# Optimization experiments

Hardware: AMD Instinct MI355X
Metric: run time of the kernel (lower is better)

## Reference

```python
import jax, jax.numpy as jnp
import numpy as np

TEMP = 0.1  # config['dsmax_temperature']


def _dual_softmax(sim):
    return jax.nn.softmax(sim, axis=1) * jax.nn.softmax(sim, axis=2)


def _pool(x, out):
    # AdaptiveAvgPool2d((out,out)) for H,W integer multiples of out
    n, c, h, w = x.shape
    return x.reshape(n, c, out, h // out, out, w // out).mean(axis=(3, 5))


def _conv1x1(w, x):
    # bias-free 1x1 conv: w [O,C], x [N,C,H,W]
    return jnp.einsum('oc,nchw->nohw', w, x)


def setup_inputs() -> dict:
    key = jax.random.key(0)
    ks = jax.random.split(key, 16)
    N = 1
    d = {}
    d['feats12_0'] = jax.random.normal(ks[0], (N, 6400, 128), jnp.float32)
    d['feats12_1'] = jax.random.normal(ks[1], (N, 6400, 128), jnp.float32)
    d['feats14_0'] = jax.random.normal(ks[2], (N, 6400, 196), jnp.float32)
    d['feats14_1'] = jax.random.normal(ks[3], (N, 6400, 196), jnp.float32)
    d['feats18_0'] = jax.random.normal(ks[4], (N, 1600, 256), jnp.float32)
    d['feats18_1'] = jax.random.normal(ks[5], (N, 1600, 256), jnp.float32)
    d['feats116_0'] = jax.random.normal(ks[6], (N, 400, 256), jnp.float32)
    d['feats116_1'] = jax.random.normal(ks[7], (N, 400, 256), jnp.float32)
    d['t1'] = jax.random.normal(ks[8], (N, 400, 256), jnp.float32)
    d['t2'] = jax.random.normal(ks[9], (N, 400, 256), jnp.float32)
    d['t3'] = jax.random.normal(ks[10], (N, 100, 196), jnp.float32)
    d['t4'] = jax.random.normal(ks[11], (N, 25, 128), jnp.float32)
    d['W_down1_16'] = jax.random.normal(ks[12], (256, 768), jnp.float32) * 0.02
    d['W_down1_8'] = jax.random.normal(ks[13], (256, 512), jnp.float32) * 0.02
    d['W_downt3'] = jax.random.normal(ks[14], (128, 1100), jnp.float32) * 0.02
    d['W_downt4'] = jax.random.normal(ks[15], (128, 256), jnp.float32) * 0.02
    return d


def reference(feats12_0, feats12_1, feats14_0, feats14_1, feats18_0, feats18_1,
              feats116_0, feats116_1, t1, t2, t3, t4,
              W_down1_16, W_down1_8, W_downt3, W_downt4):
    N = feats116_0.shape[0]
    # --- 1/16 scale: dual-softmax match + argmax gather (bug-faithful: last batch's argmax reused for all batches) ---
    conf116 = _dual_softmax(jnp.einsum('nlc,nsc->nls', feats116_0, feats116_1))
    f116_1g = feats116_1[:, jnp.argmax(conf116, axis=-1)[-1]]  # gather [L116]
    feats116 = jnp.concatenate([feats116_0, f116_1g], axis=-1).reshape(N, 20, 20, 512).transpose(0, 3, 1, 2)
    t2_img = t2.reshape(N, 20, 20, t1.shape[2]).transpose(0, 3, 1, 2)
    t2_ = _conv1x1(W_down1_16, jnp.concatenate([t2_img, feats116], axis=1))  # [N,256,20,20]
    # --- 1/8 scale ---
    conf18 = _dual_softmax(jnp.einsum('nmd,nkd->nmk', feats18_0, feats18_1))
    f18_1g = feats18_1[:, jnp.argmax(conf18, axis=-1)[-1]]
    feats18 = jnp.concatenate([feats18_0, f18_1g], axis=-1).reshape(N, 40, 40, 512).transpose(0, 3, 1, 2)
    feats18 = _pool(_conv1x1(W_down1_8, feats18), 10)  # [N,256,10,10]
    t2p = _pool(t2_, 10)                               # [N,256,10,10]
    t3_img = t3.reshape(N, 10, 10, t3.shape[2]).transpose(0, 3, 1, 2)  # [N,196,10,10]
    # --- 1/4 scale ---
    conf14 = _dual_softmax(jnp.einsum('nlc,nsc->nls', feats14_0, feats14_1))
    f14_1g = feats14_1[:, jnp.argmax(conf14, axis=-1)[-1]]
    feats14 = jnp.concatenate([feats14_0, f14_1g], axis=-1).reshape(N, 80, 80, 392).transpose(0, 3, 1, 2)
    feats14 = _pool(feats14, 10)  # [N,392,10,10]
    t3c = jnp.concatenate([t3_img, t2p, feats18, feats14], axis=1)  # [N,1100,10,10]
    t3d = _pool(_conv1x1(W_downt3, t3c), 5)  # [N,128,5,5]
    t4_img = t4.reshape(N, 5, 5, 128).transpose(0, 3, 1, 2)
    t4d = _conv1x1(W_downt4, jnp.concatenate([t3d, t4_img], axis=1))  # [N,128,5,5]
    t4seq = t4d.reshape(N, 128, 25).transpose(0, 2, 1)  # [N,25,128]
    # --- fine scale: topic routing + dual-softmax matching ---
    feats12 = jnp.concatenate([feats12_0, feats12_1], axis=1)  # [N,2L,128]
    dmatrix12 = jnp.einsum('nmd,nkd->nmk', feats12, t4seq)     # [N,2L,25]
    topic_idx = jnp.argmax(dmatrix12, axis=-1)                 # one-hot scatter == argmax routing
    # einsum('nmhd,nlsd->nhs') of the one-hot-routed tensors sums over topics;
    # since one-hot rows sum to 1 over topics, it equals the direct contraction:
    conf12 = _dual_softmax(jnp.einsum('nld,nsd->nls', feats12_0, feats12_1)) / TEMP
    mask12 = (conf12 > 1.0).astype(conf12.dtype)
    conf12 = conf12 * mask12  # nonzero entries give index_i / index_j
    return conf18, conf12, topic_idx
```

## Files before the change

kernel.cpp:

```cpp
#include <hip/hip_runtime.h>
#include <math.h>

#define TPB 256
#define C0F 20.0f

typedef __attribute__((ext_vector_type(4))) float f32x4;
typedef short s16x8 __attribute__((ext_vector_type(8)));

static inline int cdiv(int a, int b) { return (a + b - 1) / b; }

#define GLOAD_LDS16(g, l)                                                        \
  __builtin_amdgcn_global_load_lds(                                              \
      (const __attribute__((address_space(1))) unsigned int*)(const void*)(g),   \
      (__attribute__((address_space(3))) unsigned int*)(void*)(l), 16, 0, 0)

__device__ __forceinline__ unsigned short f2bf_rne(float f) {
  unsigned int u = __float_as_uint(f);
  return (unsigned short)((u + 0x7FFFu + ((u >> 16) & 1u)) >> 16);
}
__device__ __forceinline__ float bf2f(unsigned short h) {
  return __uint_as_float(((unsigned int)h) << 16);
}

__global__ __launch_bounds__(TPB) void pack_split2(const float* __restrict__ XA,
                                                   const float* __restrict__ XB,
                                                   unsigned short* __restrict__ outA,
                                                   unsigned short* __restrict__ outB,
                                                   int M, int D, int K2p,
                                                   int codesA, int codesB) {
  int id = blockIdx.x * TPB + threadIdx.x;
  if (id >= M * K2p) return;
  const float* X = blockIdx.y ? XB : XA;
  unsigned short* out = blockIdx.y ? outB : outA;
  int codes = blockIdx.y ? codesB : codesA;
  int m = id / K2p, k = id - m * K2p;
  int s = k / D;
  unsigned short v = 0;
  if (s < 6) {
    int d = k - s * D;
    float a = X[(size_t)m * D + d];
    unsigned short h = f2bf_rne(a);
    int code = (codes >> (2 * s)) & 3;
    if (code == 0) {
      v = h;
    } else {
      float r1 = a - bf2f(h);
      unsigned short mi = f2bf_rne(r1);
      if (code == 1) v = mi;
      else v = f2bf_rne(r1 - bf2f(mi));
    }
  }
  out[id] = v;
}

template <bool EXACT, bool ROWSTATS>
__global__ __launch_bounds__(TPB) void gemm_bf16_nt(const unsigned short* __restrict__ A,
                                                    const unsigned short* __restrict__ B,
                                                    float* __restrict__ C,
                                                    int M, int N, int K, int gx, int gy,
                                                    float* __restrict__ cps,
                                                    float* __restrict__ rps) {
  __shared__ __align__(16) unsigned short As[128 * 64];
  __shared__ __align__(16) unsigned short Bs[128 * 64];
  const int tid = threadIdx.x;
  const int lane = tid & 63;
  const int w = tid >> 6;
  const int wm = w >> 1, wn = w & 1;

  const int nwg = gridDim.x;
  const int q = nwg >> 3, r = nwg & 7;
  const int xcd = blockIdx.x & 7, pos = blockIdx.x >> 3;
  const int wgid = (xcd < r ? xcd * (q + 1) : r * (q + 1) + (xcd - r) * q) + pos;
  const int tpg = 8 * gx;
  const int g = wgid / tpg;
  const int rem = wgid - g * tpg;
  const int rows = min(8, gy - g * 8);
  const int bx = rem / rows;
  const int by = g * 8 + rem - bx * rows;
  const int bm = by * 128, bn = bx * 128;

  f32x4 acc[4][4];
#pragma unroll
  for (int m = 0; m < 4; ++m)
#pragma unroll
    for (int n = 0; n < 4; ++n) acc[m][n] = (f32x4){0.f, 0.f, 0.f, 0.f};

  const unsigned short* gA[4];
  const unsigned short* gB[4];
#pragma unroll
  for (int i = 0; i < 4; ++i) {
    int qq = (w * 4 + i) * 64 + lane;
    int rr = qq >> 3;
    int cc = (qq & 7) ^ (rr & 7);
    int ga = bm + rr, gb = bn + rr;
    if (!EXACT) { if (ga >= M) ga = M - 1; if (gb >= N) gb = N - 1; }
    gA[i] = A + (size_t)ga * K + cc * 8;
    gB[i] = B + (size_t)gb * K + cc * 8;
  }

  for (int k0 = 0; k0 < K; k0 += 64) {
#pragma unroll
    for (int i = 0; i < 4; ++i) {
      GLOAD_LDS16(gA[i] + k0, As + (w * 4 + i) * 512);
      GLOAD_LDS16(gB[i] + k0, Bs + (w * 4 + i) * 512);
    }
    __syncthreads();
#pragma unroll
    for (int ks = 0; ks < 2; ++ks) {
      s16x8 af[4], bfr[4];
      const int c0 = ks * 4 + (lane >> 4);
#pragma unroll
      for (int m = 0; m < 4; ++m) {
        int ra = wm * 64 + m * 16 + (lane & 15);
        af[m] = *(const s16x8*)(As + ra * 64 + ((c0 ^ (ra & 7)) * 8));
        int rb = wn * 64 + m * 16 + (lane & 15);
        bfr[m] = *(const s16x8*)(Bs + rb * 64 + ((c0 ^ (rb & 7)) * 8));
      }
#pragma unroll
      for (int m = 0; m < 4; ++m)
#pragma unroll
        for (int n = 0; n < 4; ++n)
          acc[m][n] = __builtin_amdgcn_mfma_f32_16x16x32_bf16(af[m], bfr[n], acc[m][n], 0, 0, 0);
    }
    __syncthreads();
  }

#pragma unroll
  for (int m = 0; m < 4; ++m) {
    int row0 = bm + wm * 64 + m * 16 + (lane >> 4) * 4;
#pragma unroll
    for (int n = 0; n < 4; ++n) {
      int col = bn + wn * 64 + n * 16 + (lane & 15);
      if (EXACT || col < N) {
#pragma unroll
        for (int j = 0; j < 4; ++j) {
          int r2 = row0 + j;
          if (EXACT || r2 < M) C[(size_t)r2 * N + col] = acc[m][n][j];
        }
      }
    }
  }

#pragma unroll
  for (int m = 0; m < 4; ++m)
#pragma unroll
    for (int n = 0; n < 4; ++n)
#pragma unroll
      for (int j = 0; j < 4; ++j) acc[m][n][j] = __expf(acc[m][n][j] - C0F);

  float* scs = (float*)As;
  const int slot = wm * 4 + (lane >> 4);
#pragma unroll
  for (int n = 0; n < 4; ++n) {
    int lcol = wn * 64 + n * 16 + (lane & 15);
    float s = 0.f;
#pragma unroll
    for (int m = 0; m < 4; ++m)
#pragma unroll
      for (int j = 0; j < 4; ++j) {
        if (!EXACT) {
          int grow = bm + wm * 64 + m * 16 + (lane >> 4) * 4 + j;
          if (grow >= M) continue;
        }
        s += acc[m][n][j];
      }
    scs[slot * 128 + lcol] = s;
  }
  __syncthreads();
  if (tid < 128) {
    float s = 0.f;
#pragma unroll
    for (int k = 0; k < 8; ++k) s += scs[k * 128 + tid];
    if (EXACT || bn + tid < N) cps[(size_t)by * N + bn + tid] = s;
  }

  if (ROWSTATS) {
    float* srs = (float*)Bs;
#pragma unroll
    for (int m = 0; m < 4; ++m)
#pragma unroll
      for (int j = 0; j < 4; ++j) {
        float s = 0.f;
#pragma unroll
        for (int n = 0; n < 4; ++n) {
          if (!EXACT) {
            int gcol = bn + wn * 64 + n * 16 + (lane & 15);
            if (gcol >= N) continue;
          }
          s += acc[m][n][j];
        }
#pragma unroll
        for (int d = 1; d < 16; d <<= 1) s += __shfl_xor(s, d);
        if ((lane & 15) == 0) srs[wn * 128 + wm * 64 + m * 16 + (lane >> 4) * 4 + j] = s;
      }
    __syncthreads();
    if (tid < 128) {
      float s = srs[tid] + srs[128 + tid];
      if (EXACT || bm + tid < M) rps[(size_t)bx * M + bm + tid] = s;
    }
  }
}

template <bool ROWSTATS>
__global__ __launch_bounds__(512) void gemm_big(const unsigned short* __restrict__ A,
                                                const unsigned short* __restrict__ B,
                                                float* __restrict__ C,
                                                int M, int N, int K, int gx, int gy,
                                                float* __restrict__ cps,
                                                float* __restrict__ rps) {
  __shared__ __align__(16) unsigned short As[128 * 64];
  __shared__ __align__(16) unsigned short Bs[256 * 64];
  const int tid = threadIdx.x;
  const int lane = tid & 63;
  const int w = tid >> 6;
  const int wm = w >> 2, wn = w & 3;

  const int nwg = gridDim.x;
  const int q = nwg >> 3, r = nwg & 7;
  const int xcd = blockIdx.x & 7, pos = blockIdx.x >> 3;
  const int wgid = (xcd < r ? xcd * (q + 1) : r * (q + 1) + (xcd - r) * q) + pos;
  const int tpg = 8 * gx;
  const int g = wgid / tpg;
  const int rem = wgid - g * tpg;
  const int rows = min(8, gy - g * 8);
  const int bx = rem / rows;
  const int by = g * 8 + rem - bx * rows;
  const int bm = by * 128, bn = bx * 256;

  f32x4 acc[4][4];
#pragma unroll
  for (int m = 0; m < 4; ++m)
#pragma unroll
    for (int n = 0; n < 4; ++n) acc[m][n] = (f32x4){0.f, 0.f, 0.f, 0.f};

  const unsigned short* gA[2];
  const unsigned short* gB[4];
#pragma unroll
  for (int i = 0; i < 2; ++i) {
    int qq = i * 512 + tid;
    int rr = qq >> 3;
    int cc = (qq & 7) ^ (rr & 7);
    gA[i] = A + (size_t)(bm + rr) * K + cc * 8;
  }
#pragma unroll
  for (int i = 0; i < 4; ++i) {
    int qq = i * 512 + tid;
    int rr = qq >> 3;
    int cc = (qq & 7) ^ (rr & 7);
    gB[i] = B + (size_t)(bn + rr) * K + cc * 8;
  }

  for (int k0 = 0; k0 < K; k0 += 64) {
#pragma unroll
    for (int i = 0; i < 2; ++i)
      GLOAD_LDS16(gA[i] + k0, As + (i * 8 + w) * 512);
#pragma unroll
    for (int i = 0; i < 4; ++i)
      GLOAD_LDS16(gB[i] + k0, Bs + (i * 8 + w) * 512);
    __syncthreads();
#pragma unroll
    for (int ks = 0; ks < 2; ++ks) {
      s16x8 af[4], bfr[4];
      const int c0 = ks * 4 + (lane >> 4);
#pragma unroll
      for (int m = 0; m < 4; ++m) {
        int ra = wm * 64 + m * 16 + (lane & 15);
        af[m] = *(const s16x8*)(As + ra * 64 + ((c0 ^ (ra & 7)) * 8));
        int rb = wn * 64 + m * 16 + (lane & 15);
        bfr[m] = *(const s16x8*)(Bs + rb * 64 + ((c0 ^ (rb & 7)) * 8));
      }
#pragma unroll
      for (int m = 0; m < 4; ++m)
#pragma unroll
        for (int n = 0; n < 4; ++n)
          acc[m][n] = __builtin_amdgcn_mfma_f32_16x16x32_bf16(af[m], bfr[n], acc[m][n], 0, 0, 0);
    }
    __syncthreads();
  }

#pragma unroll
  for (int m = 0; m < 4; ++m) {
    int row0 = bm + wm * 64 + m * 16 + (lane >> 4) * 4;
#pragma unroll
    for (int n = 0; n < 4; ++n) {
      int col = bn + wn * 64 + n * 16 + (lane & 15);
#pragma unroll
      for (int j = 0; j < 4; ++j)
        C[(size_t)(row0 + j) * N + col] = acc[m][n][j];
    }
  }

#pragma unroll
  for (int m = 0; m < 4; ++m)
#pragma unroll
    for (int n = 0; n < 4; ++n)
#pragma unroll
      for (int j = 0; j < 4; ++j) acc[m][n][j] = __expf(acc[m][n][j] - C0F);

  float* scs = (float*)As;
  const int slot = wm * 4 + (lane >> 4);
#pragma unroll
  for (int n = 0; n < 4; ++n) {
    int lcol = wn * 64 + n * 16 + (lane & 15);
    float s = 0.f;
#pragma unroll
    for (int m = 0; m < 4; ++m)
#pragma unroll
      for (int j = 0; j < 4; ++j) s += acc[m][n][j];
    scs[slot * 256 + lcol] = s;
  }
  __syncthreads();
  if (tid < 256) {
    float s = 0.f;
#pragma unroll
    for (int k = 0; k < 8; ++k) s += scs[k * 256 + tid];
    cps[(size_t)by * N + bn + tid] = s;
  }

  if (ROWSTATS) {
    float* srs = (float*)Bs;
#pragma unroll
    for (int m = 0; m < 4; ++m)
#pragma unroll
      for (int j = 0; j < 4; ++j) {
        float s = 0.f;
#pragma unroll
        for (int n = 0; n < 4; ++n) s += acc[m][n][j];
#pragma unroll
        for (int d = 1; d < 16; d <<= 1) s += __shfl_xor(s, d);
        if ((lane & 15) == 0) srs[wn * 128 + wm * 64 + m * 16 + (lane >> 4) * 4 + j] = s;
      }
    __syncthreads();
    if (tid < 128) {
      float s = (srs[tid] + srs[128 + tid]) + (srs[256 + tid] + srs[384 + tid]);
      rps[(size_t)bx * M + bm + tid] = s;
    }
  }
}

__global__ __launch_bounds__(TPB) void logsum_combine2(const float* __restrict__ cps,
                                                       const float* __restrict__ rps,
                                                       int S, int nch_c, int nch_r,
                                                       float* __restrict__ out_c,
                                                       float* __restrict__ out_r) {
  int s = blockIdx.x * TPB + threadIdx.x;
  if (s >= S) return;
  const float* ps = blockIdx.y ? rps : cps;
  int nch = blockIdx.y ? nch_r : nch_c;
  float a = 0.f;
  for (int c = 0; c < nch; ++c) a += ps[(size_t)c * S + s];
  (blockIdx.y ? out_r : out_c)[s] = logf(a);
}

__global__ __launch_bounds__(TPB) void finalize_argmax(const float* __restrict__ sim, int S,
                                                       const float* __restrict__ pen,
                                                       int* __restrict__ amax) {
  __shared__ float rv[TPB];
  __shared__ int ri[TPB];
  const int l = blockIdx.x;
  const f32x4* row = (const f32x4*)(sim + (size_t)l * S);
  const f32x4* pv = (const f32x4*)pen;
  float bv = -INFINITY;
  int bi = 0;
  for (int j4 = threadIdx.x; j4 < (S >> 2); j4 += TPB) {
    f32x4 v = row[j4];
    f32x4 p = pv[j4];
#pragma unroll
    for (int k = 0; k < 4; ++k) {
      float sc = 2.f * v[k] - p[k];
      if (sc > bv) { bv = sc; bi = j4 * 4 + k; }
    }
  }
  rv[threadIdx.x] = bv;
  ri[threadIdx.x] = bi;
  __syncthreads();
  for (int stp = TPB / 2; stp > 0; stp >>= 1) {
    if (threadIdx.x < stp) {
      float v2 = rv[threadIdx.x + stp];
      int i2 = ri[threadIdx.x + stp];
      if (v2 > rv[threadIdx.x] || (v2 == rv[threadIdx.x] && i2 < ri[threadIdx.x])) {
        rv[threadIdx.x] = v2;
        ri[threadIdx.x] = i2;
      }
    }
    __syncthreads();
  }
  if (threadIdx.x == 0) amax[l] = ri[0];
}

__global__ __launch_bounds__(TPB) void finalize_write(float* __restrict__ sim, int S,
                                                      const float* __restrict__ cls,
                                                      const float* __restrict__ rls,
                                                      int* __restrict__ amax) {
  __shared__ float rv[TPB];
  __shared__ int ri[TPB];
  const int l = blockIdx.x;
  const float rl = rls[l] + 2.0f * C0F;
  f32x4* row = (f32x4*)(sim + (size_t)l * S);
  const f32x4* cv = (const f32x4*)cls;
  float bv = -INFINITY;
  int bi = 0;
  for (int j4 = threadIdx.x; j4 < (S >> 2); j4 += TPB) {
    f32x4 v = row[j4];
    f32x4 cl = cv[j4];
    f32x4 o;
#pragma unroll
    for (int k = 0; k < 4; ++k) {
      float conf = expf(2.f * v[k] - cl[k] - rl);
      o[k] = conf;
      if (conf > bv) { bv = conf; bi = j4 * 4 + k; }
    }
    row[j4] = o;
  }
  rv[threadIdx.x] = bv;
  ri[threadIdx.x] = bi;
  __syncthreads();
  for (int stp = TPB / 2; stp > 0; stp >>= 1) {
    if (threadIdx.x < stp) {
      float v2 = rv[threadIdx.x + stp];
      int i2 = ri[threadIdx.x + stp];
      if (v2 > rv[threadIdx.x] || (v2 == rv[threadIdx.x] && i2 < ri[threadIdx.x])) {
        rv[threadIdx.x] = v2;
        ri[threadIdx.x] = i2;
      }
    }
    __syncthreads();
  }
  if (threadIdx.x == 0) amax[l] = ri[0];
}

__global__ __launch_bounds__(TPB) void finalize_mask(float* __restrict__ sim, int S,
                                                     const float* __restrict__ cls,
                                                     const float* __restrict__ rls) {
  const int l = blockIdx.x;
  const float rl = rls[l] + 2.0f * C0F - 2.302585093f;
  f32x4* row = (f32x4*)(sim + (size_t)l * S);
  const f32x4* cv = (const f32x4*)cls;
  for (int j4 = threadIdx.x; j4 < (S >> 2); j4 += TPB) {
    f32x4 v = row[j4];
    f32x4 cl = cv[j4];
    f32x4 o;
#pragma unroll
    for (int k = 0; k < 4; ++k) {
      float c = expf(2.f * v[k] - cl[k] - rl);
      o[k] = (c > 1.0f) ? c : 0.0f;
    }
    row[j4] = o;
  }
}

__global__ void build_x16(const float* __restrict__ t2, const float* __restrict__ f0,
                          const float* __restrict__ f1, const int* __restrict__ idx,
                          float* __restrict__ X) {
  int id = blockIdx.x * TPB + threadIdx.x;
  if (id >= 768 * 400) return;
  int c = id / 400, p = id % 400;
  float v;
  if (c < 256) v = t2[p * 256 + c];
  else if (c < 512) v = f0[p * 256 + (c - 256)];
  else v = f1[idx[p] * 256 + (c - 512)];
  X[id] = v;
}

__global__ void build_x8(const float* __restrict__ f0, const float* __restrict__ f1,
                         const int* __restrict__ idx, float* __restrict__ X) {
  int id = blockIdx.x * TPB + threadIdx.x;
  if (id >= 512 * 1600) return;
  int c = id / 1600, p = id % 1600;
  float v = (c < 256) ? f0[p * 256 + c] : f1[idx[p] * 256 + (c - 256)];
  X[id] = v;
}

__global__ __launch_bounds__(TPB) void conv1x1_v2(const float* __restrict__ W,
                                                  const float* __restrict__ X,
                                                  float* __restrict__ Y,
                                                  int O, int C, int P) {
  __shared__ float red[TPB];
  const int o = blockIdx.y;
  const int pl = threadIdx.x & 63;
  const int p = blockIdx.x * 64 + pl;
  const int cg = threadIdx.x >> 6;
  const float* wr = W + (size_t)o * C;
  float a0 = 0.f, a1 = 0.f, a2 = 0.f, a3 = 0.f;
  if (p < P) {
    int c = cg;
    for (; c + 12 < C; c += 16) {
      a0 += wr[c]      * X[(size_t)c * P + p];
      a1 += wr[c + 4]  * X[(size_t)(c + 4) * P + p];
      a2 += wr[c + 8]  * X[(size_t)(c + 8) * P + p];
      a3 += wr[c + 12] * X[(size_t)(c + 12) * P + p];
    }
    for (; c < C; c += 4) a0 += wr[c] * X[(size_t)c * P + p];
  }
  red[threadIdx.x] = (a0 + a1) + (a2 + a3);
  __syncthreads();
  if (threadIdx.x < 64) {
    float s = (red[threadIdx.x] + red[threadIdx.x + 64]) +
              (red[threadIdx.x + 128] + red[threadIdx.x + 192]);
    if (p < P) Y[(size_t)o * P + p] = s;
  }
}

__global__ void pool_k(const float* __restrict__ in, float* __restrict__ out, int C, int H, int f) {
  int h = H / f;
  int id = blockIdx.x * TPB + threadIdx.x;
  if (id >= C * h * h) return;
  int c = id / (h * h);
  int r = id % (h * h);
  int py = r / h, px = r % h;
  float s = 0.f;
  for (int i = 0; i < f; ++i)
    for (int j = 0; j < f; ++j)
      s += in[(size_t)c * H * H + (size_t)(py * f + i) * H + (px * f + j)];
  out[id] = s / (float)(f * f);
}

__global__ void pool14(const float* __restrict__ f0, const float* __restrict__ f1,
                       const int* __restrict__ idx, float* __restrict__ out) {
  int id = blockIdx.x * TPB + threadIdx.x;
  if (id >= 392 * 100) return;
  int c = id / 100;
  int r = id % 100;
  int py = r / 10, px = r % 10;
  float s = 0.f;
  for (int i = 0; i < 8; ++i)
    for (int j = 0; j < 8; ++j) {
      int p = (py * 8 + i) * 80 + (px * 8 + j);
      float v = (c < 196) ? f0[p * 196 + c] : f1[idx[p] * 196 + (c - 196)];
      s += v;
    }
  out[id] = s * (1.0f / 64.0f);
}

__global__ void build_xt3(const float* __restrict__ t3, const float* __restrict__ t2p,
                          const float* __restrict__ f18p, const float* __restrict__ f14p,
                          float* __restrict__ X) {
  int id = blockIdx.x * TPB + threadIdx.x;
  if (id >= 1100 * 100) return;
  int c = id / 100, p = id % 100;
  float v;
  if (c < 196) v = t3[p * 196 + c];
  else if (c < 452) v = t2p[(c - 196) * 100 + p];
  else if (c < 708) v = f18p[(c - 452) * 100 + p];
  else v = f14p[(c - 708) * 100 + p];
  X[id] = v;
}

__global__ void build_xt4(const float* __restrict__ t3d, const float* __restrict__ t4,
                          float* __restrict__ X) {
  int id = blockIdx.x * TPB + threadIdx.x;
  if (id >= 256 * 25) return;
  int c = id / 25, p = id % 25;
  X[id] = (c < 128) ? t3d[c * 25 + p] : t4[p * 128 + (c - 128)];
}

__global__ __launch_bounds__(TPB) void topic_k(const float* __restrict__ f0, const float* __restrict__ f1,
                                               const float* __restrict__ t4d, float* __restrict__ out) {
  __shared__ float s_t4[25 * 128];
  for (int i = threadIdx.x; i < 25 * 128; i += TPB) {
    int k = i >> 7, d = i & 127;
    s_t4[i] = t4d[d * 25 + k];
  }
  __syncthreads();
  int m = blockIdx.x * TPB + threadIdx.x;
  if (m >= 12800) return;
  const f32x4* row = (const f32x4*)((m < 6400) ? (f0 + (size_t)m * 128)
                                               : (f1 + (size_t)(m - 6400) * 128));
  float acc[25];
#pragma unroll
  for (int k = 0; k < 25; ++k) acc[k] = 0.f;
  for (int d4 = 0; d4 < 32; ++d4) {
    f32x4 x = row[d4];
#pragma unroll
    for (int k = 0; k < 25; ++k) {
      const float* t = s_t4 + k * 128 + d4 * 4;
      acc[k] += x[0] * t[0] + x[1] * t[1] + x[2] * t[2] + x[3] * t[3];
    }
  }
  int best = 0;
  float bv = acc[0];
#pragma unroll
  for (int k = 1; k < 25; ++k)
    if (acc[k] > bv) { bv = acc[k]; best = k; }
  out[m] = (float)best;
}

extern "C" void kernel_launch(void* const* d_in, const int* in_sizes, int n_in,
                              void* d_out, int out_size, void* d_ws, size_t ws_size,
                              hipStream_t stream) {
  const float* f12_0 = (const float*)d_in[0];
  const float* f12_1 = (const float*)d_in[1];
  const float* f14_0 = (const float*)d_in[2];
  const float* f14_1 = (const float*)d_in[3];
  const float* f18_0 = (const float*)d_in[4];
  const float* f18_1 = (const float*)d_in[5];
  const float* f116_0 = (const float*)d_in[6];
  const float* f116_1 = (const float*)d_in[7];
  const float* t2 = (const float*)d_in[9];
  const float* t3 = (const float*)d_in[10];
  const float* t4 = (const float*)d_in[11];
  const float* W16 = (const float*)d_in[12];
  const float* W8 = (const float*)d_in[13];
  const float* Wt3 = (const float*)d_in[14];
  const float* Wt4 = (const float*)d_in[15];

  float* out = (float*)d_out;
  float* conf18 = out;
  float* conf12 = out + 2560000;
  float* topic = out + 2560000 + 40960000;

  float* w = (float*)d_ws;
  auto alloc = [&](size_t n) { float* p = w; w += ((n + 63) & ~(size_t)63); return p; };

  unsigned short* pA = (unsigned short*)alloc(6400 * 1216 / 2);
  unsigned short* pB = (unsigned short*)alloc(6400 * 1216 / 2);
  float* sim116 = alloc(400 * 400);
  float* pen116 = alloc(400);
  int* idx116 = (int*)alloc(400);
  float* cls18 = alloc(1600); float* rls18 = alloc(1600);
  int* idx18 = (int*)alloc(1600);
  float* pen14 = alloc(6400);
  int* idx14 = (int*)alloc(6400);
  float* cls12 = alloc(6400); float* rls12 = alloc(6400);
  float* cps = alloc(50 * 6400);
  float* rps = alloc(50 * 6400);
  float* X16 = alloc(768 * 400);
  float* t2_ = alloc(256 * 400);
  float* X8 = alloc(512 * 1600);
  float* conv18b = alloc(256 * 1600);
  float* f18p = alloc(256 * 100);
  float* t2p = alloc(256 * 100);
  float* f14p = alloc(392 * 100);
  float* Xt3 = alloc(1100 * 100);
  float* t3conv = alloc(128 * 100);
  float* t3d = alloc(128 * 25);
  float* Xt4 = alloc(256 * 25);
  float* t4d = alloc(128 * 25);

  const int CA = 0 | (0 << 2) | (1 << 4) | (0 << 6) | (2 << 8) | (1 << 10);
  const int CB = 0 | (1 << 2) | (0 << 4) | (2 << 6) | (0 << 8) | (1 << 10);

  {
    int L = 400, S = 400, K2 = 1536;
    int gx = cdiv(S, 128), gy = cdiv(L, 128);
    pack_split2<<<dim3(cdiv(L * K2, TPB), 2), TPB, 0, stream>>>(f116_0, f116_1, pA, pB, L, 256, K2, CA, CB);
    gemm_bf16_nt<false, false><<<gx * gy, TPB, 0, stream>>>(pA, pB, sim116, L, S, K2, gx, gy,
                                                            cps, nullptr);
    logsum_combine2<<<dim3(cdiv(S, TPB), 1), TPB, 0, stream>>>(cps, nullptr, S, gy, 0, pen116, nullptr);
    finalize_argmax<<<L, TPB, 0, stream>>>(sim116, S, pen116, idx116);
  }

  build_x16<<<cdiv(768 * 400, TPB), TPB, 0, stream>>>(t2, f116_0, f116_1, idx116, X16);
  conv1x1_v2<<<dim3(cdiv(400, 64), 256), TPB, 0, stream>>>(W16, X16, t2_, 256, 768, 400);

  {
    int L = 1600, S = 1600, K2 = 1536;
    int gx = cdiv(S, 128), gy = cdiv(L, 128);
    pack_split2<<<dim3(cdiv(L * K2, TPB), 2), TPB, 0, stream>>>(f18_0, f18_1, pA, pB, L, 256, K2, CA, CB);
    gemm_bf16_nt<false, true><<<gx * gy, TPB, 0, stream>>>(pA, pB, conf18, L, S, K2, gx, gy,
                                                           cps, rps);
    logsum_combine2<<<dim3(cdiv(S, TPB), 2), TPB, 0, stream>>>(cps, rps, S, gy, gx, cls18, rls18);
    finalize_write<<<L, TPB, 0, stream>>>(conf18, S, cls18, rls18, idx18);
  }

  build_x8<<<cdiv(512 * 1600, TPB), TPB, 0, stream>>>(f18_0, f18_1, idx18, X8);
  conv1x1_v2<<<dim3(cdiv(1600, 64), 256), TPB, 0, stream>>>(W8, X8, conv18b, 256, 512, 1600);
  pool_k<<<cdiv(256 * 100, TPB), TPB, 0, stream>>>(conv18b, f18p, 256, 40, 4);
  pool_k<<<cdiv(256 * 100, TPB), TPB, 0, stream>>>(t2_, t2p, 256, 20, 2);

  {
    int L = 6400, S = 6400, K2 = 1216;
    int gx = cdiv(S, 256), gy = cdiv(L, 128);
    pack_split2<<<dim3(cdiv(L * K2, TPB), 2), TPB, 0, stream>>>(f14_0, f14_1, pA, pB, L, 196, K2, CA, CB);
    gemm_big<false><<<gx * gy, 512, 0, stream>>>(pA, pB, conf12, L, S, K2, gx, gy,
                                                 cps, nullptr);
    logsum_combine2<<<dim3(cdiv(S, TPB), 1), TPB, 0, stream>>>(cps, nullptr, S, gy, 0, pen14, nullptr);
    finalize_argmax<<<L, TPB, 0, stream>>>(conf12, S, pen14, idx14);
  }
  pool14<<<cdiv(392 * 100, TPB), TPB, 0, stream>>>(f14_0, f14_1, idx14, f14p);

  build_xt3<<<cdiv(1100 * 100, TPB), TPB, 0, stream>>>(t3, t2p, f18p, f14p, Xt3);
  conv1x1_v2<<<dim3(cdiv(100, 64), 128), TPB, 0, stream>>>(Wt3, Xt3, t3conv, 128, 1100, 100);
  pool_k<<<cdiv(128 * 25, TPB), TPB, 0, stream>>>(t3conv, t3d, 128, 10, 2);

  build_xt4<<<cdiv(256 * 25, TPB), TPB, 0, stream>>>(t3d, t4, Xt4);
  conv1x1_v2<<<dim3(cdiv(25, 64), 128), TPB, 0, stream>>>(Wt4, Xt4, t4d, 128, 256, 25);

  topic_k<<<cdiv(12800, TPB), TPB, 0, stream>>>(f12_0, f12_1, t4d, topic);

  {
    int L = 6400, S = 6400, K2 = 768;
    int gx = cdiv(S, 256), gy = cdiv(L, 128);
    pack_split2<<<dim3(cdiv(L * K2, TPB), 2), TPB, 0, stream>>>(f12_0, f12_1, pA, pB, L, 128, K2, CA, CB);
    gemm_big<true><<<gx * gy, 512, 0, stream>>>(pA, pB, conf12, L, S, K2, gx, gy,
                                                cps, rps);
    logsum_combine2<<<dim3(cdiv(S, TPB), 2), TPB, 0, stream>>>(cps, rps, S, gy, gx, cls12, rls12);
    finalize_mask<<<L, TPB, 0, stream>>>(conf12, S, cls12, rls12);
  }
}
```

Before: 611.5 us.

## Double-buffer gemm_big LDS tiles with K-step 32 and column-major layout

Changes gemm_big's main loop from a single-buffered K=64 tile to a double-buffered K=32 tile. The next tile's global-to-LDS load is issued before the current tile's MFMAs, so memory latency overlaps with compute. The LDS layout changes to chunk-major (k-chunk, row) instead of XOR-swizzled row-major, and a min-waves-per-EU hint is added to launch_bounds. It keeps one barrier per iteration. The risks are more loop iterations with half the work each, possible LDS bank conflicts from the new layout, and register pressure from the occupancy hint.

```diff
diff --git a/kernel.cpp b/kernel.cpp
--- a/kernel.cpp
+++ b/kernel.cpp
@@ -202,14 +202,14 @@
 }
 
 template <bool ROWSTATS>
-__global__ __launch_bounds__(512) void gemm_big(const unsigned short* __restrict__ A,
-                                                const unsigned short* __restrict__ B,
-                                                float* __restrict__ C,
-                                                int M, int N, int K, int gx, int gy,
-                                                float* __restrict__ cps,
-                                                float* __restrict__ rps) {
-  __shared__ __align__(16) unsigned short As[128 * 64];
-  __shared__ __align__(16) unsigned short Bs[256 * 64];
+__global__ __launch_bounds__(512, 6) void gemm_big(const unsigned short* __restrict__ A,
+                                                   const unsigned short* __restrict__ B,
+                                                   float* __restrict__ C,
+                                                   int M, int N, int K, int gx, int gy,
+                                                   float* __restrict__ cps,
+                                                   float* __restrict__ rps) {
+  __shared__ __align__(16) unsigned short As[2][128 * 32];
+  __shared__ __align__(16) unsigned short Bs[2][256 * 32];
   const int tid = threadIdx.x;
   const int lane = tid & 63;
   const int w = tid >> 6;
@@ -233,41 +233,37 @@
 #pragma unroll
     for (int n = 0; n < 4; ++n) acc[m][n] = (f32x4){0.f, 0.f, 0.f, 0.f};
 
-  const unsigned short* gA[2];
-  const unsigned short* gB[4];
-#pragma unroll
-  for (int i = 0; i < 2; ++i) {
-    int qq = i * 512 + tid;
-    int rr = qq >> 3;
-    int cc = (qq & 7) ^ (rr & 7);
-    gA[i] = A + (size_t)(bm + rr) * K + cc * 8;
-  }
-#pragma unroll
-  for (int i = 0; i < 4; ++i) {
-    int qq = i * 512 + tid;
-    int rr = qq >> 3;
-    int cc = (qq & 7) ^ (rr & 7);
-    gB[i] = B + (size_t)(bn + rr) * K + cc * 8;
-  }
-
-  for (int k0 = 0; k0 < K; k0 += 64) {
-#pragma unroll
-    for (int i = 0; i < 2; ++i)
-      GLOAD_LDS16(gA[i] + k0, As + (i * 8 + w) * 512);
-#pragma unroll
-    for (int i = 0; i < 4; ++i)
-      GLOAD_LDS16(gB[i] + k0, Bs + (i * 8 + w) * 512);
-    __syncthreads();
-#pragma unroll
-    for (int ks = 0; ks < 2; ++ks) {
+  const int qa = tid;
+  const unsigned aoff = (unsigned)(bm + (qa & 127)) * (unsigned)K + (unsigned)((qa >> 7) * 8);
+  const int qb0 = tid, qb1 = 512 + tid;
+  const unsigned boff0 = (unsigned)(bn + (qb0 & 255)) * (unsigned)K + (unsigned)((qb0 >> 8) * 8);
+  const unsigned boff1 = (unsigned)(bn + (qb1 & 255)) * (unsigned)K + (unsigned)((qb1 >> 8) * 8);
+
+  const int nt = K >> 5;
+  int cur = 0;
+
+  GLOAD_LDS16(A + aoff, &As[0][0] + (size_t)(w * 64) * 8);
+  GLOAD_LDS16(B + boff0, &Bs[0][0] + (size_t)(w * 64) * 8);
+  GLOAD_LDS16(B + boff1, &Bs[0][0] + (size_t)(512 + w * 64) * 8);
+  __syncthreads();
+
+  for (int t = 0; t < nt; ++t) {
+    if (t + 1 < nt) {
+      unsigned ko = (unsigned)((t + 1) << 5);
+      int nxt = cur ^ 1;
+      GLOAD_LDS16(A + (aoff + ko), &As[nxt][0] + (size_t)(w * 64) * 8);
+      GLOAD_LDS16(B + (boff0 + ko), &Bs[nxt][0] + (size_t)(w * 64) * 8);
+      GLOAD_LDS16(B + (boff1 + ko), &Bs[nxt][0] + (size_t)(512 + w * 64) * 8);
+    }
+    {
       s16x8 af[4], bfr[4];
-      const int c0 = ks * 4 + (lane >> 4);
+      const int c0 = lane >> 4;
 #pragma unroll
       for (int m = 0; m < 4; ++m) {
         int ra = wm * 64 + m * 16 + (lane & 15);
-        af[m] = *(const s16x8*)(As + ra * 64 + ((c0 ^ (ra & 7)) * 8));
+        af[m] = *(const s16x8*)(&As[cur][0] + ((size_t)(c0 * 128 + ra)) * 8);
         int rb = wn * 64 + m * 16 + (lane & 15);
-        bfr[m] = *(const s16x8*)(Bs + rb * 64 + ((c0 ^ (rb & 7)) * 8));
+        bfr[m] = *(const s16x8*)(&Bs[cur][0] + ((size_t)(c0 * 256 + rb)) * 8);
       }
 #pragma unroll
       for (int m = 0; m < 4; ++m)
@@ -276,6 +272,7 @@
           acc[m][n] = __builtin_amdgcn_mfma_f32_16x16x32_bf16(af[m], bfr[n], acc[m][n], 0, 0, 0);
     }
     __syncthreads();
+    cur ^= 1;
   }
 
 #pragma unroll
@@ -297,7 +294,7 @@
 #pragma unroll
       for (int j = 0; j < 4; ++j) acc[m][n][j] = __expf(acc[m][n][j] - C0F);
 
-  float* scs = (float*)As;
+  float* scs = (float*)&As[0][0];
   const int slot = wm * 4 + (lane >> 4);
 #pragma unroll
   for (int n = 0; n < 4; ++n) {
@@ -318,7 +315,7 @@
   }
 
   if (ROWSTATS) {
-    float* srs = (float*)Bs;
+    float* srs = (float*)&Bs[0][0];
 #pragma unroll
     for (int m = 0; m < 4; ++m)
 #pragma unroll
```

Result: slower. 1.492 ms (+144.0%).

## Fuse concat/gather builds into conv1x1 kernels, merge pools, split topic reduction

Applied to the files above, without the earlier changes.

Removes the separate build_x* kernels that materialised concatenated/gathered channel-major inputs, and has each 1x1 conv read directly from the source tensors (including the argmax-gathered rows). The two adaptive pools are merged into one launch, and the topic routing kernel now splits the 128-dim dot across four thread groups with a shared-memory reduction, giving it 200 blocks instead of 50. This cuts launches and intermediate global traffic. The trade-off is that the fused conv reads row-major inputs with a per-thread stride, so its loads are no longer coalesced across lanes.

```diff
diff --git a/kernel.cpp b/kernel.cpp
--- a/kernel.cpp
+++ b/kernel.cpp
@@ -449,55 +449,124 @@
   }
 }
 
-__global__ void build_x16(const float* __restrict__ t2, const float* __restrict__ f0,
-                          const float* __restrict__ f1, const int* __restrict__ idx,
-                          float* __restrict__ X) {
-  int id = blockIdx.x * TPB + threadIdx.x;
-  if (id >= 768 * 400) return;
-  int c = id / 400, p = id % 400;
-  float v;
-  if (c < 256) v = t2[p * 256 + c];
-  else if (c < 512) v = f0[p * 256 + (c - 256)];
-  else v = f1[idx[p] * 256 + (c - 512)];
-  X[id] = v;
-}
-
-__global__ void build_x8(const float* __restrict__ f0, const float* __restrict__ f1,
-                         const int* __restrict__ idx, float* __restrict__ X) {
-  int id = blockIdx.x * TPB + threadIdx.x;
-  if (id >= 512 * 1600) return;
-  int c = id / 1600, p = id % 1600;
-  float v = (c < 256) ? f0[p * 256 + c] : f1[idx[p] * 256 + (c - 256)];
-  X[id] = v;
-}
-
-__global__ __launch_bounds__(TPB) void conv1x1_v2(const float* __restrict__ W,
-                                                  const float* __restrict__ X,
-                                                  float* __restrict__ Y,
-                                                  int O, int C, int P) {
+__global__ __launch_bounds__(TPB) void conv16_f(const float* __restrict__ W,
+                                                const float* __restrict__ t2,
+                                                const float* __restrict__ f0,
+                                                const float* __restrict__ f1,
+                                                const int* __restrict__ idx,
+                                                float* __restrict__ Y) {
   __shared__ float red[TPB];
   const int o = blockIdx.y;
   const int pl = threadIdx.x & 63;
   const int p = blockIdx.x * 64 + pl;
   const int cg = threadIdx.x >> 6;
-  const float* wr = W + (size_t)o * C;
-  float a0 = 0.f, a1 = 0.f, a2 = 0.f, a3 = 0.f;
-  if (p < P) {
-    int c = cg;
-    for (; c + 12 < C; c += 16) {
-      a0 += wr[c]      * X[(size_t)c * P + p];
-      a1 += wr[c + 4]  * X[(size_t)(c + 4) * P + p];
-      a2 += wr[c + 8]  * X[(size_t)(c + 8) * P + p];
-      a3 += wr[c + 12] * X[(size_t)(c + 12) * P + p];
-    }
-    for (; c < C; c += 4) a0 += wr[c] * X[(size_t)c * P + p];
-  }
-  red[threadIdx.x] = (a0 + a1) + (a2 + a3);
+  const float* wr = W + (size_t)o * 768;
+  float a = 0.f;
+  if (p < 400) {
+    int ip = idx[p];
+    const float* r0 = t2 + p * 256;
+    const float* r1 = f0 + p * 256;
+    const float* r2 = f1 + ip * 256;
+    for (int c = cg; c < 256; c += 4) {
+      a += wr[c] * r0[c];
+      a += wr[c + 256] * r1[c];
+      a += wr[c + 512] * r2[c];
+    }
+  }
+  red[threadIdx.x] = a;
   __syncthreads();
   if (threadIdx.x < 64) {
     float s = (red[threadIdx.x] + red[threadIdx.x + 64]) +
               (red[threadIdx.x + 128] + red[threadIdx.x + 192]);
-    if (p < P) Y[(size_t)o * P + p] = s;
+    if (p < 400) Y[(size_t)o * 400 + p] = s;
+  }
+}
+
+__global__ __launch_bounds__(TPB) void conv8_f(const float* __restrict__ W,
+                                               const float* __restrict__ f0,
+                                               const float* __restrict__ f1,
+                                               const int* __restrict__ idx,
+                                               float* __restrict__ Y) {
+  __shared__ float red[TPB];
+  const int o = blockIdx.y;
+  const int pl = threadIdx.x & 63;
+  const int p = blockIdx.x * 64 + pl;
+  const int cg = threadIdx.x >> 6;
+  const float* wr = W + (size_t)o * 512;
+  float a = 0.f;
+  if (p < 1600) {
+    int ip = idx[p];
+    const float* r0 = f0 + p * 256;
+    const float* r1 = f1 + ip * 256;
+    for (int c = cg; c < 256; c += 4) {
+      a += wr[c] * r0[c];
+      a += wr[c + 256] * r1[c];
+    }
+  }
+  red[threadIdx.x] = a;
+  __syncthreads();
+  if (threadIdx.x < 64) {
+    float s = (red[threadIdx.x] + red[threadIdx.x + 64]) +
+              (red[threadIdx.x + 128] + red[threadIdx.x + 192]);
+    if (p < 1600) Y[(size_t)o * 1600 + p] = s;
+  }
+}
+
+__global__ __launch_bounds__(TPB) void convt3_f(const float* __restrict__ W,
+                                                const float* __restrict__ t3,
+                                                const float* __restrict__ t2p,
+                                                const float* __restrict__ f18p,
+                                                const float* __restrict__ f14p,
+                                                float* __restrict__ Y) {
+  __shared__ float red[TPB];
+  const int o = blockIdx.y;
+  const int pl = threadIdx.x & 63;
+  const int p = blockIdx.x * 64 + pl;
+  const int cg = threadIdx.x >> 6;
+  const float* wr = W + (size_t)o * 1100;
+  float a = 0.f;
+  if (p < 100) {
+    const float* r0 = t3 + p * 196;
+    for (int c = cg; c < 196; c += 4) a += wr[c] * r0[c];
+    for (int c = cg; c < 256; c += 4) {
+      a += wr[196 + c] * t2p[c * 100 + p];
+      a += wr[452 + c] * f18p[c * 100 + p];
+    }
+    for (int c = cg; c < 392; c += 4) a += wr[708 + c] * f14p[c * 100 + p];
+  }
+  red[threadIdx.x] = a;
+  __syncthreads();
+  if (threadIdx.x < 64) {
+    float s = (red[threadIdx.x] + red[threadIdx.x + 64]) +
+              (red[threadIdx.x + 128] + red[threadIdx.x + 192]);
+    if (p < 100) Y[(size_t)o * 100 + p] = s;
+  }
+}
+
+__global__ __launch_bounds__(TPB) void convt4_f(const float* __restrict__ W,
+                                                const float* __restrict__ t3d,
+                                                const float* __restrict__ t4,
+                                                float* __restrict__ Y) {
+  __shared__ float red[TPB];
+  const int o = blockIdx.y;
+  const int pl = threadIdx.x & 63;
+  const int p = blockIdx.x * 64 + pl;
+  const int cg = threadIdx.x >> 6;
+  const float* wr = W + (size_t)o * 256;
+  float a = 0.f;
+  if (p < 25) {
+    const float* r1 = t4 + p * 128;
+    for (int c = cg; c < 128; c += 4) {
+      a += wr[c] * t3d[c * 25 + p];
+      a += wr[128 + c] * r1[c];
+    }
+  }
+  red[threadIdx.x] = a;
+  __syncthreads();
+  if (threadIdx.x < 64) {
+    float s = (red[threadIdx.x] + red[threadIdx.x + 64]) +
+              (red[threadIdx.x + 128] + red[threadIdx.x + 192]);
+    if (p < 25) Y[(size_t)o * 25 + p] = s;
   }
 }
 
@@ -513,6 +582,28 @@
     for (int j = 0; j < f; ++j)
       s += in[(size_t)c * H * H + (size_t)(py * f + i) * H + (px * f + j)];
   out[id] = s / (float)(f * f);
+}
+
+__global__ void pool_pair(const float* __restrict__ in0, const float* __restrict__ in1,
+                          float* __restrict__ out0, float* __restrict__ out1) {
+  int id = blockIdx.x * TPB + threadIdx.x;
+  if (id >= 256 * 100) return;
+  int c = id / 100;
+  int r = id % 100;
+  int py = r / 10, px = r % 10;
+  if (blockIdx.y == 0) {
+    float s = 0.f;
+    for (int i = 0; i < 4; ++i)
+      for (int j = 0; j < 4; ++j)
+        s += in0[(size_t)c * 1600 + (size_t)(py * 4 + i) * 40 + (px * 4 + j)];
+    out0[id] = s * 0.0625f;
+  } else {
+    float s = 0.f;
+    for (int i = 0; i < 2; ++i)
+      for (int j = 0; j < 2; ++j)
+        s += in1[(size_t)c * 400 + (size_t)(py * 2 + i) * 20 + (px * 2 + j)];
+    out1[id] = s * 0.25f;
+  }
 }
 
 __global__ void pool14(const float* __restrict__ f0, const float* __restrict__ f1,
@@ -532,57 +623,47 @@
   out[id] = s * (1.0f / 64.0f);
 }
 
-__global__ void build_xt3(const float* __restrict__ t3, const float* __restrict__ t2p,
-                          const float* __restrict__ f18p, const float* __restrict__ f14p,
-                          float* __restrict__ X) {
-  int id = blockIdx.x * TPB + threadIdx.x;
-  if (id >= 1100 * 100) return;
-  int c = id / 100, p = id % 100;
-  float v;
-  if (c < 196) v = t3[p * 196 + c];
-  else if (c < 452) v = t2p[(c - 196) * 100 + p];
-  else if (c < 708) v = f18p[(c - 452) * 100 + p];
-  else v = f14p[(c - 708) * 100 + p];
-  X[id] = v;
-}
-
-__global__ void build_xt4(const float* __restrict__ t3d, const float* __restrict__ t4,
-                          float* __restrict__ X) {
-  int id = blockIdx.x * TPB + threadIdx.x;
-  if (id >= 256 * 25) return;
-  int c = id / 25, p = id % 25;
-  X[id] = (c < 128) ? t3d[c * 25 + p] : t4[p * 128 + (c - 128)];
-}
-
-__global__ __launch_bounds__(TPB) void topic_k(const float* __restrict__ f0, const float* __restrict__ f1,
-                                               const float* __restrict__ t4d, float* __restrict__ out) {
+__global__ __launch_bounds__(TPB) void topic_k4(const float* __restrict__ f0,
+                                                const float* __restrict__ f1,
+                                                const float* __restrict__ t4d,
+                                                float* __restrict__ out) {
   __shared__ float s_t4[25 * 128];
+  __shared__ float red[4 * 64 * 25];
   for (int i = threadIdx.x; i < 25 * 128; i += TPB) {
     int k = i >> 7, d = i & 127;
     s_t4[i] = t4d[d * 25 + k];
   }
   __syncthreads();
-  int m = blockIdx.x * TPB + threadIdx.x;
-  if (m >= 12800) return;
+  const int r = threadIdx.x & 63;
+  const int gq = threadIdx.x >> 6;
+  const int m = blockIdx.x * 64 + r;
   const f32x4* row = (const f32x4*)((m < 6400) ? (f0 + (size_t)m * 128)
                                                : (f1 + (size_t)(m - 6400) * 128));
   float acc[25];
 #pragma unroll
   for (int k = 0; k < 25; ++k) acc[k] = 0.f;
-  for (int d4 = 0; d4 < 32; ++d4) {
-    f32x4 x = row[d4];
+  for (int d4 = 0; d4 < 8; ++d4) {
+    f32x4 x = row[gq * 8 + d4];
 #pragma unroll
     for (int k = 0; k < 25; ++k) {
-      const float* t = s_t4 + k * 128 + d4 * 4;
+      const float* t = s_t4 + k * 128 + (gq * 8 + d4) * 4;
       acc[k] += x[0] * t[0] + x[1] * t[1] + x[2] * t[2] + x[3] * t[3];
     }
   }
-  int best = 0;
-  float bv = acc[0];
-#pragma unroll
-  for (int k = 1; k < 25; ++k)
-    if (acc[k] > bv) { bv = acc[k]; best = k; }
-  out[m] = (float)best;
+#pragma unroll
+  for (int k = 0; k < 25; ++k) red[(gq * 64 + r) * 25 + k] = acc[k];
+  __syncthreads();
+  if (gq == 0) {
+    int best = 0;
+    float bv = -INFINITY;
+#pragma unroll
+    for (int k = 0; k < 25; ++k) {
+      float s = (red[r * 25 + k] + red[(64 + r) * 25 + k]) +
+                (red[(128 + r) * 25 + k] + red[(192 + r) * 25 + k]);
+      if (s > bv) { bv = s; best = k; }
+    }
+    out[m] = (float)best;
+  }
 }
 
 extern "C" void kernel_launch(void* const* d_in, const int* in_sizes, int n_in,
@@ -624,17 +705,13 @@
   float* cls12 = alloc(6400); float* rls12 = alloc(6400);
   float* cps = alloc(50 * 6400);
   float* rps = alloc(50 * 6400);
-  float* X16 = alloc(768 * 400);
   float* t2_ = alloc(256 * 400);
-  float* X8 = alloc(512 * 1600);
   float* conv18b = alloc(256 * 1600);
   float* f18p = alloc(256 * 100);
   float* t2p = alloc(256 * 100);
   float* f14p = alloc(392 * 100);
-  float* Xt3 = alloc(1100 * 100);
   float* t3conv = alloc(128 * 100);
   float* t3d = alloc(128 * 25);
-  float* Xt4 = alloc(256 * 25);
   float* t4d = alloc(128 * 25);
 
   const int CA = 0 | (0 << 2) | (1 << 4) | (0 << 6) | (2 << 8) | (1 << 10);
@@ -650,8 +727,7 @@
     finalize_argmax<<<L, TPB, 0, stream>>>(sim116, S, pen116, idx116);
   }
 
-  build_x16<<<cdiv(768 * 400, TPB), TPB, 0, stream>>>(t2, f116_0, f116_1, idx116, X16);
-  conv1x1_v2<<<dim3(cdiv(400, 64), 256), TPB, 0, stream>>>(W16, X16, t2_, 256, 768, 400);
+  conv16_f<<<dim3(cdiv(400, 64), 256), TPB, 0, stream>>>(W16, t2, f116_0, f116_1, idx116, t2_);
 
   {
     int L = 1600, S = 1600, K2 = 1536;
@@ -663,10 +739,8 @@
     finalize_write<<<L, TPB, 0, stream>>>(conf18, S, cls18, rls18, idx18);
   }
 
-  build_x8<<<cdiv(512 * 1600, TPB), TPB, 0, stream>>>(f18_0, f18_1, idx18, X8);
-  conv1x1_v2<<<dim3(cdiv(1600, 64), 256), TPB, 0, stream>>>(W8, X8, conv18b, 256, 512, 1600);
-  pool_k<<<cdiv(256 * 100, TPB), TPB, 0, stream>>>(conv18b, f18p, 256, 40, 4);
-  pool_k<<<cdiv(256 * 100, TPB), TPB, 0, stream>>>(t2_, t2p, 256, 20, 2);
+  conv8_f<<<dim3(cdiv(1600, 64), 256), TPB, 0, stream>>>(W8, f18_0, f18_1, idx18, conv18b);
+  pool_pair<<<dim3(cdiv(256 * 100, TPB), 2), TPB, 0, stream>>>(conv18b, t2_, f18p, t2p);
 
   {
     int L = 6400, S = 6400, K2 = 1216;
@@ -679,14 +753,12 @@
   }
   pool14<<<cdiv(392 * 100, TPB), TPB, 0, stream>>>(f14_0, f14_1, idx14, f14p);
 
-  build_xt3<<<cdiv(1100 * 100, TPB), TPB, 0, stream>>>(t3, t2p, f18p, f14p, Xt3);
-  conv1x1_v2<<<dim3(cdiv(100, 64), 128), TPB, 0, stream>>>(Wt3, Xt3, t3conv, 128, 1100, 100);
+  convt3_f<<<dim3(cdiv(100, 64), 128), TPB, 0, stream>>>(Wt3, t3, t2p, f18p, f14p, t3conv);
   pool_k<<<cdiv(128 * 25, TPB), TPB, 0, stream>>>(t3conv, t3d, 128, 10, 2);
 
-  build_xt4<<<cdiv(256 * 25, TPB), TPB, 0, stream>>>(t3d, t4, Xt4);
-  conv1x1_v2<<<dim3(cdiv(25, 64), 128), TPB, 0, stream>>>(Wt4, Xt4, t4d, 128, 256, 25);
-
-  topic_k<<<cdiv(12800, TPB), TPB, 0, stream>>>(f12_0, f12_1, t4d, topic);
+  convt4_f<<<dim3(1, 128), TPB, 0, stream>>>(Wt4, t3d, t4, t4d);
+
+  topic_k4<<<200, TPB, 0, stream>>>(f12_0, f12_1, t4d, topic);
 
   {
     int L = 6400, S = 6400, K2 = 768;
```

After: 1.290 ms. 111% more time.
